# Optimization experiments

Hardware: AMD Instinct MI355X
Metric: run time of the kernel (lower is better)

The kernel has to match this reference:

```python
import jax, jax.numpy as jnp
import numpy as np

HEAD_DIM = 64
EMB_DIM = 768
BATCH = 4
SEQ = 4096

def setup_inputs() -> dict:
    key = jax.random.key(0)
    ks = jax.random.split(key, 7)
    s = 1.0 / np.sqrt(EMB_DIM)
    return {
        "X": jax.random.normal(ks[0], (BATCH, SEQ, EMB_DIM), dtype=jnp.float32),
        "Wq": jax.random.uniform(ks[1], (EMB_DIM, HEAD_DIM), jnp.float32, -s, s),
        "bq": jax.random.uniform(ks[2], (HEAD_DIM,), jnp.float32, -s, s),
        "Wk": jax.random.uniform(ks[3], (EMB_DIM, HEAD_DIM), jnp.float32, -s, s),
        "bk": jax.random.uniform(ks[4], (HEAD_DIM,), jnp.float32, -s, s),
        "Wv": jax.random.uniform(ks[5], (EMB_DIM, HEAD_DIM), jnp.float32, -s, s),
        "bv": jax.random.uniform(ks[6], (HEAD_DIM,), jnp.float32, -s, s),
    }

def reference(X, Wq, bq, Wk, bk, Wv, bv):
    # X: (B, S, E)
    B, S, E = X.shape
    q = X @ Wq + bq  # (B, S, D)
    k = X @ Wk + bk
    v = X @ Wv + bv
    scores = jnp.einsum("bsd,btd->bst", q, k)  # (B, S, S)
    # Original masks with -inf BEFORE scaling; -inf/sqrt(d) stays -inf,
    # so equivalent to: mask then scale.
    causal = jnp.tril(jnp.ones((S, S), dtype=bool))
    scores = jnp.where(causal, scores, -jnp.inf) / jnp.sqrt(jnp.float32(q.shape[-1]))
    w = jax.nn.softmax(scores, axis=-1)
    # dropout_rate = 0.0 (eval-equivalent): identity
    return jnp.einsum("bst,btd->bsd", w, v)
```

## Files before the change

### kernel.cpp

```cpp
#include <hip/hip_runtime.h>
#include <stdint.h>


#define QSCALE 0.18033688011112042f

using short4v = __attribute__((ext_vector_type(4))) short;
using short8v = __attribute__((ext_vector_type(8))) short;
using float4v = __attribute__((ext_vector_type(4))) float;
using uint4v  = __attribute__((ext_vector_type(4))) unsigned int;
typedef unsigned long long ull;
typedef unsigned short ushort;

#if __has_builtin(__builtin_amdgcn_exp2f)
#define EXP2F(x) __builtin_amdgcn_exp2f(x)
#else
#define EXP2F(x) exp2f(x)
#endif

__device__ __forceinline__ ushort f2b(float f) {
  union { float f; unsigned u; } cv; cv.f = f;
  unsigned u = cv.u;
  u += 0x7FFFu + ((u >> 16) & 1u);
  return (ushort)(u >> 16);
}
__device__ __forceinline__ ushort f2h(float f) {
  union { ushort u; _Float16 h; } cv; cv.h = (_Float16)f;
  return cv.u;
}
__device__ __forceinline__ float h2f(unsigned u16) {
  union { ushort u; _Float16 h; } cv; cv.u = (ushort)u16;
  return (float)cv.h;
}

__global__ void wpack_kernel(const float* __restrict__ Wq, const float* __restrict__ bq,
                             const float* __restrict__ Wk, const float* __restrict__ bk,
                             const float* __restrict__ Wv, const float* __restrict__ bv,
                             ushort* __restrict__ Wt, float* __restrict__ bb) {
  __shared__ float tile[64 * 65];
  const int t = threadIdx.x;
  const int m = blockIdx.x % 3, e0 = (blockIdx.x / 3) * 64;
  const float* Wsrc = (m == 0) ? Wq : (m == 1) ? Wk : Wv;
  const float sc = (m == 0) ? QSCALE : 1.0f;
#pragma unroll
  for (int i = 0; i < 16; ++i) {
    int idx = i * 256 + t, n = idx & 63, el = idx >> 6;
    tile[el * 65 + n] = Wsrc[(size_t)(e0 + el) * 64 + n];
  }
  __syncthreads();
#pragma unroll
  for (int i = 0; i < 16; ++i) {
    int idx = i * 256 + t, el = idx & 63, n = idx >> 6;
    Wt[(size_t)(m * 64 + n) * 768 + e0 + el] = f2b(tile[el * 65 + n] * sc);
  }
  if (blockIdx.x == 0 && t < 192) {
    float bvv;
    if (t < 64)       bvv = bq[t] * QSCALE;
    else if (t < 128) bvv = bk[t - 64];
    else              bvv = bv[t - 128];
    bb[t] = bvv;
  }
}

__global__ __launch_bounds__(256, 4) void proj_kernel(
    const float* __restrict__ X, const ushort* __restrict__ Wt,
    const float* __restrict__ bb,
    ushort* __restrict__ Qb, ushort* __restrict__ Kb, ushort* __restrict__ Vt) {
  const int t = threadIdx.x;
  const int wv = t >> 6, lane = t & 63, g = lane >> 4, r = lane & 15;
  const int row0 = blockIdx.x * 32;

  float4v acc[3][2];
#pragma unroll
  for (int ct = 0; ct < 3; ++ct) {
    float bias = bb[wv * 48 + ct * 16 + r];
#pragma unroll
    for (int rt = 0; rt < 2; ++rt) acc[ct][rt] = {bias, bias, bias, bias};
  }

  const float* xb = X + (size_t)(row0 + r) * 768 + g * 8;
  const ushort* wb = Wt + (size_t)(wv * 48 + r) * 768 + g * 8;

#pragma unroll 2
  for (int kc = 0; kc < 12; ++kc) {
    const int k0 = kc * 64;
    short8v af[2][2];
#pragma unroll
    for (int rt = 0; rt < 2; ++rt)
#pragma unroll
      for (int ks = 0; ks < 2; ++ks) {
        const float* xp = xb + rt * 16 * 768 + k0 + ks * 32;
        float4v x0 = *(const float4v*)xp;
        float4v x1 = *(const float4v*)(xp + 4);
        short8v v;
        v[0] = (short)f2b(x0[0]); v[1] = (short)f2b(x0[1]);
        v[2] = (short)f2b(x0[2]); v[3] = (short)f2b(x0[3]);
        v[4] = (short)f2b(x1[0]); v[5] = (short)f2b(x1[1]);
        v[6] = (short)f2b(x1[2]); v[7] = (short)f2b(x1[3]);
        af[rt][ks] = v;
      }
#pragma unroll
    for (int ct = 0; ct < 3; ++ct) {
      short8v b0 = *(const short8v*)(wb + ct * 16 * 768 + k0);
      short8v b1 = *(const short8v*)(wb + ct * 16 * 768 + k0 + 32);
#pragma unroll
      for (int rt = 0; rt < 2; ++rt) {
        acc[ct][rt] = __builtin_amdgcn_mfma_f32_16x16x32_bf16(af[rt][0], b0, acc[ct][rt], 0, 0, 0);
        acc[ct][rt] = __builtin_amdgcn_mfma_f32_16x16x32_bf16(af[rt][1], b1, acc[ct][rt], 0, 0, 0);
      }
    }
  }
#pragma unroll
  for (int ct = 0; ct < 3; ++ct) {
    int n = wv * 48 + ct * 16 + r;
    int mtx = n >> 6, dl = n & 63;
#pragma unroll
    for (int rt = 0; rt < 2; ++rt) {
#pragma unroll
      for (int i = 0; i < 4; ++i) {
        int rg = row0 + rt * 16 + g * 4 + i;
        ushort hv = f2b(acc[ct][rt][i]);
        if (mtx == 0)      Qb[rg * 64 + dl] = hv;
        else if (mtx == 1) Kb[rg * 64 + dl] = hv;
        else               Vt[(size_t)(((rg >> 12) << 6) + dl) * 4096 + (rg & 4095)] = hv;
      }
    }
  }
}

__global__ __launch_bounds__(512) void attn_kernel(
    const ushort* __restrict__ Qb, const ushort* __restrict__ Kb,
    const ushort* __restrict__ Vt, ushort* __restrict__ pacc,
    float* __restrict__ pml) {
  __shared__ char lds[32768];
  char* lk = lds;
  char* lv = lds + 16384;
  const int t = threadIdx.x;
  const int wv = t >> 6, lane = t & 63, g = lane >> 4, r = lane & 15;
  const int bx = blockIdx.x;
  const int b = bx / 144;
  const int j = 143 - (bx - b * 144);
  int a = 0;
  while (2 * (a + 1) * (a + 2) <= j) ++a;
  const int rm = j - 2 * a * (a + 1);
  const int m_ = rm / (a + 1);
  const int c = rm - m_ * (a + 1);
  const int st = 4 * a + m_;

  const int s0 = c * 32;
  const int smax = min(32, 8 * st + 8 - s0);
  const int nm = smax >> 2;
  const int qt = 8 * st + wv;
  const int mysteps = min(qt + 1 - s0, smax);
  const int dloc = qt - s0;

  const size_t qoff = ((size_t)(b * 4096 + st * 128 + wv * 16 + r)) * 64 + g * 8;
  const short8v qf0 = *(const short8v*)(Qb + qoff);
  const short8v qf1 = *(const short8v*)(Qb + qoff + 32);

  float4v acc[4];
#pragma unroll
  for (int dt = 0; dt < 4; ++dt) acc[dt] = {0.f, 0.f, 0.f, 0.f};
  float mrun = -3.0e38f, lsum = 0.f;

  const int u = t & 255, kr = u >> 2, sq = u & 3;
  const bool isK = t >= 256;
  const ushort* src;
  int wo0, wo1, sx = 0;
  if (isK) {
    src = Kb + ((size_t)(b * 4096 + c * 512 + kr)) * 64 + sq * 16;
    wo0 = (kr * 128 + sq * 32) ^ ((kr & 7) << 4);
    wo1 = wo0 ^ 16;
  } else {
    src = Vt + ((size_t)(b * 64 + kr)) * 4096 + c * 512 + sq * 16;
    wo0 = sq * 2048 + kr * 32;
    wo1 = 0;
    sx = ((kr >> 2) & 3) ^ sq;
  }

  uint4v rA0, rA1, rB0, rB1;
  auto stload = [&](int m, uint4v& v0, uint4v& v1) {
    const ushort* p = src + (isK ? (size_t)m * 4096 : (size_t)m * 64);
    v0 = *(const uint4v*)p;
    v1 = *(const uint4v*)(p + 8);
  };
  auto stwrite = [&](int bi, uint4v v0, uint4v v1) {
    if (isK) {
      *(uint4v*)(lk + bi * 8192 + wo0) = v0;
      *(uint4v*)(lk + bi * 8192 + wo1) = v1;
    } else {
      char* vb = lv + bi * 8192 + wo0;
      *(ull*)(vb + ((0 ^ sx) & 3) * 8) = (ull)v0[0] | ((ull)v0[1] << 32);
      *(ull*)(vb + ((1 ^ sx) & 3) * 8) = (ull)v0[2] | ((ull)v0[3] << 32);
      *(ull*)(vb + ((2 ^ sx) & 3) * 8) = (ull)v1[0] | ((ull)v1[1] << 32);
      *(ull*)(vb + ((3 ^ sx) & 3) * 8) = (ull)v1[2] | ((ull)v1[3] << 32);
    }
  };

  auto micro = [&](int bi, int ks, bool masked) {
    const char* lkb = lk + bi * 8192;
    const char* lvb = lv + bi * 8192 + ks * 2048;
    const int krow = ks * 16 + r;
    const int rsw = (r & 7) << 4;
    const short8v k0 = *(const short8v*)(lkb + ((krow * 128 + g * 16) ^ rsw));
    const short8v k1 = *(const short8v*)(lkb + ((krow * 128 + g * 16 + 64) ^ rsw));
    float4v s = {0.f, 0.f, 0.f, 0.f};
    __builtin_amdgcn_s_setprio(1);
    s = __builtin_amdgcn_mfma_f32_16x16x32_bf16(k0, qf0, s, 0, 0, 0);
    s = __builtin_amdgcn_mfma_f32_16x16x32_bf16(k1, qf1, s, 0, 0, 0);
    __builtin_amdgcn_s_setprio(0);
    float u0 = s[0], u1 = s[1], u2 = s[2], u3 = s[3];
    if (masked) {
      int k4 = g << 2;
      u0 = (k4 + 0 <= r) ? u0 : -3.0e38f;
      u1 = (k4 + 1 <= r) ? u1 : -3.0e38f;
      u2 = (k4 + 2 <= r) ? u2 : -3.0e38f;
      u3 = (k4 + 3 <= r) ? u3 : -3.0e38f;
    }
    float tmax = fmaxf(fmaxf(u0, u1), fmaxf(u2, u3));
    tmax = fmaxf(tmax, __shfl_xor(tmax, 16));
    tmax = fmaxf(tmax, __shfl_xor(tmax, 32));
    float p0, p1, p2, p3;
    if (__all(tmax <= mrun)) {
      p0 = EXP2F(u0 - mrun); p1 = EXP2F(u1 - mrun);
      p2 = EXP2F(u2 - mrun); p3 = EXP2F(u3 - mrun);
      lsum += (p0 + p1) + (p2 + p3);
    } else {
      float mn = fmaxf(mrun, tmax);
      float rs = EXP2F(mrun - mn);
      mrun = mn;
      p0 = EXP2F(u0 - mn); p1 = EXP2F(u1 - mn);
      p2 = EXP2F(u2 - mn); p3 = EXP2F(u3 - mn);
      lsum = lsum * rs + ((p0 + p1) + (p2 + p3));
#pragma unroll
      for (int dt = 0; dt < 4; ++dt) acc[dt] *= rs;
    }
    short4v pf;
    pf[0] = (short)f2b(p0); pf[1] = (short)f2b(p1);
    pf[2] = (short)f2b(p2); pf[3] = (short)f2b(p3);
    const int vsl = ((g ^ (r >> 2) ^ ks) & 3) << 3;
    __builtin_amdgcn_s_setprio(1);
#pragma unroll
    for (int dt = 0; dt < 4; ++dt) {
      const short4v vf = *(const short4v*)(lvb + (16 * dt + r) * 32 + vsl);
      acc[dt] = __builtin_amdgcn_mfma_f32_16x16x16bf16_1k(vf, pf, acc[dt], 0, 0, 0);
    }
    __builtin_amdgcn_s_setprio(0);
  };

  stload(0, rA0, rA1);
  stwrite(0, rA0, rA1);
  if (nm > 1) stload(1, rA0, rA1);
  rB0 = rA0; rB1 = rA1;
  __syncthreads();

  for (int m = 0; m < nm; ++m) {
    if (m + 2 < nm) stload(m + 2, rB0, rB1);
    const int nl = mysteps - m * 4;
    const int bi = m & 1;
    if (nl > 0) micro(bi, 0, m * 4 + 0 == dloc);
    if (nl > 1) micro(bi, 1, m * 4 + 1 == dloc);
    if (nl > 2) micro(bi, 2, m * 4 + 2 == dloc);
    if (nl > 3) micro(bi, 3, m * 4 + 3 == dloc);
    if (m + 1 < nm) stwrite((m + 1) & 1, rA0, rA1);
    __syncthreads();
    rA0 = rB0; rA1 = rB1;
  }

  lsum += __shfl_xor(lsum, 16);
  lsum += __shfl_xor(lsum, 32);

  const int slot = bx;
  const int prow = wv * 16 + r;
  if (g == 0) {
    pml[slot * 256 + prow * 2 + 0] = mrun;
    pml[slot * 256 + prow * 2 + 1] = lsum;
  }
  ushort* pp = pacc + (size_t)slot * 8192 + prow * 64;
#pragma unroll
  for (int dt = 0; dt < 4; ++dt) {
    ull pk = (ull)f2h(acc[dt][0]) | ((ull)f2h(acc[dt][1]) << 16) |
             ((ull)f2h(acc[dt][2]) << 32) | ((ull)f2h(acc[dt][3]) << 48);
    *(ull*)(pp + dt * 16 + g * 4) = pk;
  }
}

__global__ __launch_bounds__(64) void combine_kernel(
    const ushort* __restrict__ pacc, const float* __restrict__ pml,
    float* __restrict__ out) {
  const int bx = blockIdx.x;
  const int rq = bx & 31, st = (bx >> 5) & 31, b = bx >> 10;
  const int a = st >> 2, nc = a + 1;
  const int base = 2 * a * (a + 1) + (st & 3) * (a + 1);
  const int t = threadIdx.x;
  const int row = rq * 4 + (t >> 4);
  const int d0 = (t & 15) * 4;

  float M = -3.0e38f;
  for (int p = 0; p < nc; ++p) {
    int slot = b * 144 + 143 - (base + p);
    M = fmaxf(M, pml[slot * 256 + row * 2]);
  }
  float denom = 0.f;
  float4v v0 = {0.f, 0.f, 0.f, 0.f};
  for (int p = 0; p < nc; ++p) {
    int slot = b * 144 + 143 - (base + p);
    float m = pml[slot * 256 + row * 2];
    float l = pml[slot * 256 + row * 2 + 1];
    float wgt = EXP2F(m - M);
    denom += l * wgt;
    const ushort* ap = pacc + (size_t)slot * 8192 + row * 64 + d0;
    unsigned h0 = *(const unsigned*)ap;
    unsigned h1 = *(const unsigned*)(ap + 2);
    v0[0] += wgt * h2f(h0 & 0xffff); v0[1] += wgt * h2f(h0 >> 16);
    v0[2] += wgt * h2f(h1 & 0xffff); v0[3] += wgt * h2f(h1 >> 16);
  }
  float inv = 1.0f / denom;
  *(float4v*)(out + ((size_t)(b * 4096 + st * 128 + row)) * 64 + d0) = v0 * inv;
}

extern "C" void kernel_launch(void* const* d_in, const int* in_sizes, int n_in,
                              void* d_out, int out_size, void* d_ws, size_t ws_size,
                              hipStream_t stream) {
  const float* X  = (const float*)d_in[0];
  const float* Wq = (const float*)d_in[1];
  const float* bq = (const float*)d_in[2];
  const float* Wk = (const float*)d_in[3];
  const float* bk = (const float*)d_in[4];
  const float* Wv = (const float*)d_in[5];
  const float* bv = (const float*)d_in[6];
  float* out = (float*)d_out;

  ushort* Qb = (ushort*)d_ws;
  ushort* Kb = Qb + 4 * 4096 * 64;
  ushort* Vt = Kb + 4 * 4096 * 64;
  ushort* Wt = Vt + 4 * 4096 * 64;
  float* bb  = (float*)(Wt + 192 * 768);
  float* pml  = bb + 256;
  ushort* pacc = (ushort*)(pml + 576 * 256);

  wpack_kernel<<<36, 256, 0, stream>>>(Wq, bq, Wk, bk, Wv, bv, Wt, bb);
  proj_kernel<<<512, 256, 0, stream>>>(X, Wt, bb, Qb, Kb, Vt);
  attn_kernel<<<576, 512, 0, stream>>>(Qb, Kb, Vt, pacc, pml);
  combine_kernel<<<4096, 64, 0, stream>>>(pacc, pml, out);
}
```

Baseline: 174.9 us.

## Stage X tiles through swizzled double-buffered LDS and prepack W in MFMA fragment order

```diff
diff --git a/kernel.cpp b/kernel.cpp
--- a/kernel.cpp
+++ b/kernel.cpp
@@ -31,27 +31,28 @@
   union { ushort u; _Float16 h; } cv; cv.u = (ushort)u16;
   return (float)cv.h;
 }
+__device__ __forceinline__ unsigned bpk(unsigned a, unsigned b) {
+  a += 0x7FFFu + ((a >> 16) & 1u);
+  b += 0x7FFFu + ((b >> 16) & 1u);
+  return (a >> 16) | (b & 0xFFFF0000u);
+}
 
 __global__ void wpack_kernel(const float* __restrict__ Wq, const float* __restrict__ bq,
                              const float* __restrict__ Wk, const float* __restrict__ bk,
                              const float* __restrict__ Wv, const float* __restrict__ bv,
-                             ushort* __restrict__ Wt, float* __restrict__ bb) {
-  __shared__ float tile[64 * 65];
+                             ushort* __restrict__ Wf, float* __restrict__ bb) {
   const int t = threadIdx.x;
-  const int m = blockIdx.x % 3, e0 = (blockIdx.x / 3) * 64;
-  const float* Wsrc = (m == 0) ? Wq : (m == 1) ? Wk : Wv;
-  const float sc = (m == 0) ? QSCALE : 1.0f;
-#pragma unroll
-  for (int i = 0; i < 16; ++i) {
-    int idx = i * 256 + t, n = idx & 63, el = idx >> 6;
-    tile[el * 65 + n] = Wsrc[(size_t)(e0 + el) * 64 + n];
-  }
-  __syncthreads();
-#pragma unroll
-  for (int i = 0; i < 16; ++i) {
-    int idx = i * 256 + t, el = idx & 63, n = idx >> 6;
-    Wt[(size_t)(m * 64 + n) * 768 + e0 + el] = f2b(tile[el * 65 + n] * sc);
-  }
+  const int gid = blockIdx.x * 256 + t;
+  const int mtx = gid / 49152;
+  const int rem = gid - mtx * 49152;
+  const int k = rem >> 6, dl = rem & 63;
+  const float* Wsrc = (mtx == 0) ? Wq : (mtx == 1) ? Wk : Wv;
+  float val = Wsrc[rem] * ((mtx == 0) ? QSCALE : 1.0f);
+  const int n = mtx * 64 + dl;
+  const int nt = n >> 4, r = n & 15;
+  const int kc = k >> 6, k6 = k & 63;
+  const int ks = k6 >> 5, g = (k6 >> 3) & 3, j = k6 & 7;
+  Wf[(size_t)((kc * 2 + ks) * 12 + nt) * 512 + (g * 16 + r) * 8 + j] = f2b(val);
   if (blockIdx.x == 0 && t < 192) {
     float bvv;
     if (t < 64)       bvv = bq[t] * QSCALE;
@@ -61,68 +62,67 @@
   }
 }
 
-__global__ __launch_bounds__(256, 4) void proj_kernel(
-    const float* __restrict__ X, const ushort* __restrict__ Wt,
+__global__ __launch_bounds__(512) void proj_kernel(
+    const float* __restrict__ X, const ushort* __restrict__ Wf,
     const float* __restrict__ bb,
     ushort* __restrict__ Qb, ushort* __restrict__ Kb, ushort* __restrict__ Vt) {
+  __shared__ char lx[2][8192];
   const int t = threadIdx.x;
   const int wv = t >> 6, lane = t & 63, g = lane >> 4, r = lane & 15;
+  const int rh = wv >> 2, nq = wv & 3;
   const int row0 = blockIdx.x * 32;
 
-  float4v acc[3][2];
+  float4v acc[3];
 #pragma unroll
   for (int ct = 0; ct < 3; ++ct) {
-    float bias = bb[wv * 48 + ct * 16 + r];
-#pragma unroll
-    for (int rt = 0; rt < 2; ++rt) acc[ct][rt] = {bias, bias, bias, bias};
-  }
-
-  const float* xb = X + (size_t)(row0 + r) * 768 + g * 8;
-  const ushort* wb = Wt + (size_t)(wv * 48 + r) * 768 + g * 8;
-
+    float bias = bb[nq * 48 + ct * 16 + r];
+    acc[ct] = {bias, bias, bias, bias};
+  }
+
+  const int srow = t >> 4, sseg = t & 15;
+  const float* gsrc = X + (size_t)(row0 + srow) * 768 + sseg * 4;
+  const int woff = srow * 256 + ((sseg ^ (srow & 15)) << 4);
+
+  uint4v xr = *(const uint4v*)gsrc;
+  *(uint4v*)(lx[0] + woff) = xr;
+  __syncthreads();
+
+  const int rowb = (rh * 16 + r) * 256;
 #pragma unroll 2
   for (int kc = 0; kc < 12; ++kc) {
-    const int k0 = kc * 64;
-    short8v af[2][2];
-#pragma unroll
-    for (int rt = 0; rt < 2; ++rt)
-#pragma unroll
-      for (int ks = 0; ks < 2; ++ks) {
-        const float* xp = xb + rt * 16 * 768 + k0 + ks * 32;
-        float4v x0 = *(const float4v*)xp;
-        float4v x1 = *(const float4v*)(xp + 4);
-        short8v v;
-        v[0] = (short)f2b(x0[0]); v[1] = (short)f2b(x0[1]);
-        v[2] = (short)f2b(x0[2]); v[3] = (short)f2b(x0[3]);
-        v[4] = (short)f2b(x1[0]); v[5] = (short)f2b(x1[1]);
-        v[6] = (short)f2b(x1[2]); v[7] = (short)f2b(x1[3]);
-        af[rt][ks] = v;
+    if (kc < 11) xr = *(const uint4v*)(gsrc + (kc + 1) * 64);
+    const char* lb = lx[kc & 1];
+#pragma unroll
+    for (int ks = 0; ks < 2; ++ks) {
+      const int c0 = 2 * g + 8 * ks;
+      uint4v lo = *(const uint4v*)(lb + rowb + (((c0) ^ r) << 4));
+      uint4v hi = *(const uint4v*)(lb + rowb + (((c0 + 1) ^ r) << 4));
+      union { unsigned u[4]; short8v s; } a;
+      a.u[0] = bpk(lo[0], lo[1]); a.u[1] = bpk(lo[2], lo[3]);
+      a.u[2] = bpk(hi[0], hi[1]); a.u[3] = bpk(hi[2], hi[3]);
+      const ushort* wp = Wf + (size_t)((kc * 2 + ks) * 12 + nq * 3) * 512 + lane * 8;
+#pragma unroll
+      for (int ct = 0; ct < 3; ++ct) {
+        short8v bfr = *(const short8v*)(wp + ct * 512);
+        acc[ct] = __builtin_amdgcn_mfma_f32_16x16x32_bf16(a.s, bfr, acc[ct], 0, 0, 0);
       }
-#pragma unroll
-    for (int ct = 0; ct < 3; ++ct) {
-      short8v b0 = *(const short8v*)(wb + ct * 16 * 768 + k0);
-      short8v b1 = *(const short8v*)(wb + ct * 16 * 768 + k0 + 32);
-#pragma unroll
-      for (int rt = 0; rt < 2; ++rt) {
-        acc[ct][rt] = __builtin_amdgcn_mfma_f32_16x16x32_bf16(af[rt][0], b0, acc[ct][rt], 0, 0, 0);
-        acc[ct][rt] = __builtin_amdgcn_mfma_f32_16x16x32_bf16(af[rt][1], b1, acc[ct][rt], 0, 0, 0);
-      }
-    }
-  }
+    }
+    __syncthreads();
+    if (kc < 11) *(uint4v*)(lx[(kc + 1) & 1] + woff) = xr;
+    __syncthreads();
+  }
+
 #pragma unroll
   for (int ct = 0; ct < 3; ++ct) {
-    int n = wv * 48 + ct * 16 + r;
+    int n = nq * 48 + ct * 16 + r;
     int mtx = n >> 6, dl = n & 63;
 #pragma unroll
-    for (int rt = 0; rt < 2; ++rt) {
-#pragma unroll
-      for (int i = 0; i < 4; ++i) {
-        int rg = row0 + rt * 16 + g * 4 + i;
-        ushort hv = f2b(acc[ct][rt][i]);
-        if (mtx == 0)      Qb[rg * 64 + dl] = hv;
-        else if (mtx == 1) Kb[rg * 64 + dl] = hv;
-        else               Vt[(size_t)(((rg >> 12) << 6) + dl) * 4096 + (rg & 4095)] = hv;
-      }
+    for (int i = 0; i < 4; ++i) {
+      int rg = row0 + rh * 16 + g * 4 + i;
+      ushort hv = f2b(acc[ct][i]);
+      if (mtx == 0)      Qb[rg * 64 + dl] = hv;
+      else if (mtx == 1) Kb[rg * 64 + dl] = hv;
+      else               Vt[(size_t)(((rg >> 12) << 6) + dl) * 4096 + (rg & 4095)] = hv;
     }
   }
 }
@@ -333,13 +333,13 @@
   ushort* Qb = (ushort*)d_ws;
   ushort* Kb = Qb + 4 * 4096 * 64;
   ushort* Vt = Kb + 4 * 4096 * 64;
-  ushort* Wt = Vt + 4 * 4096 * 64;
-  float* bb  = (float*)(Wt + 192 * 768);
+  ushort* Wf = Vt + 4 * 4096 * 64;
+  float* bb  = (float*)(Wf + 192 * 768);
   float* pml  = bb + 256;
   ushort* pacc = (ushort*)(pml + 576 * 256);
 
-  wpack_kernel<<<36, 256, 0, stream>>>(Wq, bq, Wk, bk, Wv, bv, Wt, bb);
-  proj_kernel<<<512, 256, 0, stream>>>(X, Wt, bb, Qb, Kb, Vt);
+  wpack_kernel<<<576, 256, 0, stream>>>(Wq, bq, Wk, bk, Wv, bv, Wf, bb);
+  proj_kernel<<<512, 512, 0, stream>>>(X, Wf, bb, Qb, Kb, Vt);
   attn_kernel<<<576, 512, 0, stream>>>(Qb, Kb, Vt, pacc, pml);
   combine_kernel<<<4096, 64, 0, stream>>>(pacc, pml, out);
 }
```

New measurement: 157.0 us. 1.11x faster.
